# Kernel tuning notes

Hardware: AMD Instinct MI355X
Metric: run time of the kernel (lower is better)

## Reference

```python
import jax, jax.numpy as jnp
import numpy as np

N_NODES = 50000
N_EDGES = 800000
IN_DIM = 4
HID = 64
N_LAYERS = 3
BN_EPS = 1e-5


def setup_inputs() -> dict:
    key = jax.random.key(0)
    ks = jax.random.split(key, 16)
    x = jax.random.normal(ks[0], (N_NODES, IN_DIM), dtype=jnp.float32)
    edge_index = jax.random.randint(ks[1], (2, N_EDGES), 0, N_NODES, dtype=jnp.int32)
    # input projection
    W_in = jax.random.normal(ks[2], (IN_DIM, HID), dtype=jnp.float32) * 0.1
    b_in = jnp.zeros((HID,), dtype=jnp.float32)
    # stacked per-layer GCN weights and BatchNorm (eval-mode) params
    conv_w = jax.random.normal(ks[3], (N_LAYERS, HID, HID), dtype=jnp.float32) * 0.1
    conv_b = jnp.zeros((N_LAYERS, HID), dtype=jnp.float32)
    bn_gamma = jnp.ones((N_LAYERS, HID), dtype=jnp.float32)
    bn_beta = jnp.zeros((N_LAYERS, HID), dtype=jnp.float32)
    bn_mean = jax.random.normal(ks[4], (N_LAYERS, HID), dtype=jnp.float32) * 0.01
    bn_var = jnp.abs(jax.random.normal(ks[5], (N_LAYERS, HID), dtype=jnp.float32)) * 0.1 + 1.0
    # output projection: Linear(HID,HID) -> ReLU -> Dropout(eval: identity) -> Linear(HID,OUT)
    W1 = jax.random.normal(ks[6], (HID, HID), dtype=jnp.float32) * 0.1
    b1 = jnp.zeros((HID,), dtype=jnp.float32)
    W2 = jax.random.normal(ks[7], (HID, IN_DIM), dtype=jnp.float32) * 0.01  # xavier gain 0.1
    b2 = jnp.zeros((IN_DIM,), dtype=jnp.float32)
    return {
        "x": x, "edge_index": edge_index,
        "W_in": W_in, "b_in": b_in,
        "conv_w": conv_w, "conv_b": conv_b,
        "bn_gamma": bn_gamma, "bn_beta": bn_beta,
        "bn_mean": bn_mean, "bn_var": bn_var,
        "W1": W1, "b1": b1, "W2": W2, "b2": b2,
    }


def _gcn_graph(edge_index, n_nodes):
    """Add self loops and compute symmetric GCN normalization per edge."""
    loops = jnp.arange(n_nodes, dtype=edge_index.dtype)
    src = jnp.concatenate([edge_index[0], loops])
    dst = jnp.concatenate([edge_index[1], loops])
    deg = jax.ops.segment_sum(jnp.ones_like(dst, dtype=jnp.float32), dst,
                              num_segments=n_nodes)  # in-degree incl. self loop
    dinv = jax.lax.rsqrt(jnp.maximum(deg, 1e-12))
    enorm = dinv[src] * dinv[dst]  # [E+N]
    return src, dst, enorm


def reference(x, edge_index, W_in, b_in, conv_w, conv_b, bn_gamma, bn_beta,
              bn_mean, bn_var, W1, b1, W2, b2):
    n = x.shape[0]
    src, dst, enorm = _gcn_graph(edge_index, n)

    input_x = x
    h = x @ W_in + b_in  # [N, HID]
    for i in range(N_LAYERS):
        residual = h
        # GCNConv: linear -> normalized gather/scatter aggregate -> bias
        hw = h @ conv_w[i]
        msg = hw[src] * enorm[:, None]  # [E+N, HID] irregular gather
        h = jax.ops.segment_sum(msg, dst, num_segments=n) + conv_b[i]
        # BatchNorm1d (eval) + ReLU (dropout is identity in eval)
        h = (h - bn_mean[i]) * jax.lax.rsqrt(bn_var[i] + BN_EPS) * bn_gamma[i] + bn_beta[i]
        h = jax.nn.relu(h)
        h = h + residual  # shapes always match (HID == HID)
    # output projection MLP
    delta = jax.nn.relu(h @ W1 + b1) @ W2 + b2  # [N, IN_DIM]
    return input_x + delta
```

## Files before the change

### kernel.cpp

```cpp
#include <hip/hip_runtime.h>

#define HID 64
#define CAP 64

__device__ __forceinline__ float bf2f(unsigned short u) {
    return __uint_as_float(((unsigned)u) << 16);
}
__device__ __forceinline__ unsigned short f2bf(float f) {
    unsigned u = __float_as_uint(f);
    u += 0x7FFF + ((u >> 16) & 1);
    return (unsigned short)(u >> 16);
}

__global__ void fill_gemm(const int* __restrict__ eidx, int* __restrict__ cursor,
                          int* __restrict__ col, int E, int n, int nodes_per,
                          int chunk, int fillBlocks,
                          const float* __restrict__ x, const float* __restrict__ Win,
                          const float* __restrict__ bin, const float* __restrict__ W,
                          float* __restrict__ h, float* __restrict__ hw0) {
    if (blockIdx.x < fillBlocks) {
        int p = blockIdx.x & 7;
        int q = blockIdx.x >> 3;
        const int* __restrict__ dst = eidx + E;
        int lo = p * nodes_per;
        int hi = lo + nodes_per;
        int beg = q * chunk;
        int end = min(beg + chunk, E);
        for (int e = beg + threadIdx.x; e < end; e += 256) {
            int d = dst[e];
            if (d >= lo && d < hi) {
                int s = eidx[e];
                int pos = atomicAdd(&cursor[d], 1);
                if (pos < CAP) col[(d << 6) + pos] = s;
            }
        }
        return;
    }
    __shared__ float wl[64 * 64];
    __shared__ float winl[256];
    __shared__ float binl[64];
    __shared__ float hl[256];
    int b = blockIdx.x - fillBlocks;
    int tid = threadIdx.x;
#pragma unroll
    for (int i = 0; i < 16; ++i) wl[tid + 256 * i] = W[tid + 256 * i];
    winl[tid] = Win[tid];
    if (tid < 64) binl[tid] = bin[tid];
    int j = tid & 63;
    int w = tid >> 6;
    for (int c = 0; c < 8; ++c) {
        int v = b * 32 + c * 4 + w;
        __syncthreads();
        float hv = 0.f;
        if (v < n) {
            float4 xv = *(const float4*)&x[(size_t)v * 4];
            hv = binl[j] + xv.x * winl[j] + xv.y * winl[64 + j]
                         + xv.z * winl[128 + j] + xv.w * winl[192 + j];
            h[(size_t)v * 64 + j] = hv;
        }
        hl[tid] = hv;
        __syncthreads();
        if (v < n) {
            const float* hr = &hl[w * 64];
            float acc = 0.f;
#pragma unroll
            for (int k = 0; k < 64; ++k) acc += hr[k] * wl[k * 64 + j];
            hw0[(size_t)v * 64 + j] = acc;
        }
    }
}

__global__ void scale_k(const int* __restrict__ cursor, const float* __restrict__ hw0,
                        unsigned short* __restrict__ hws0, float* __restrict__ dinv,
                        int n) {
    int t = threadIdx.x;
    int v = blockIdx.x * 16 + (t >> 4);
    int gl = t & 15;
    if (v >= n) return;
    float di = rsqrtf((float)cursor[v] + 1.0f);
    if (gl == 0) dinv[v] = di;
    float4 a = *(const float4*)&hw0[(size_t)v * 64 + gl * 4];
    ushort4 o;
    o.x = f2bf(a.x * di);
    o.y = f2bf(a.y * di);
    o.z = f2bf(a.z * di);
    o.w = f2bf(a.w * di);
    *(ushort4*)&hws0[(size_t)v * 64 + gl * 4] = o;
}

#define GATHER_BODY(hws4, col, beg, end, s0, s1, s2, s3, gl)                      \
    {                                                                             \
        int e = beg;                                                              \
        for (; e + 7 < end; e += 8) {                                             \
            int c0 = col[e], c1 = col[e+1], c2 = col[e+2], c3 = col[e+3];         \
            int c4 = col[e+4], c5 = col[e+5], c6 = col[e+6], c7 = col[e+7];       \
            ushort4 m0 = hws4[(size_t)c0 * 16 + gl];                              \
            ushort4 m1 = hws4[(size_t)c1 * 16 + gl];                              \
            ushort4 m2 = hws4[(size_t)c2 * 16 + gl];                              \
            ushort4 m3 = hws4[(size_t)c3 * 16 + gl];                              \
            ushort4 m4 = hws4[(size_t)c4 * 16 + gl];                              \
            ushort4 m5 = hws4[(size_t)c5 * 16 + gl];                              \
            ushort4 m6 = hws4[(size_t)c6 * 16 + gl];                              \
            ushort4 m7 = hws4[(size_t)c7 * 16 + gl];                              \
            s0 += bf2f(m0.x)+bf2f(m1.x)+bf2f(m2.x)+bf2f(m3.x)                     \
                + bf2f(m4.x)+bf2f(m5.x)+bf2f(m6.x)+bf2f(m7.x);                    \
            s1 += bf2f(m0.y)+bf2f(m1.y)+bf2f(m2.y)+bf2f(m3.y)                     \
                + bf2f(m4.y)+bf2f(m5.y)+bf2f(m6.y)+bf2f(m7.y);                    \
            s2 += bf2f(m0.z)+bf2f(m1.z)+bf2f(m2.z)+bf2f(m3.z)                     \
                + bf2f(m4.z)+bf2f(m5.z)+bf2f(m6.z)+bf2f(m7.z);                    \
            s3 += bf2f(m0.w)+bf2f(m1.w)+bf2f(m2.w)+bf2f(m3.w)                     \
                + bf2f(m4.w)+bf2f(m5.w)+bf2f(m6.w)+bf2f(m7.w);                    \
        }                                                                         \
        for (; e + 3 < end; e += 4) {                                             \
            int c0 = col[e], c1 = col[e+1], c2 = col[e+2], c3 = col[e+3];         \
            ushort4 m0 = hws4[(size_t)c0 * 16 + gl];                              \
            ushort4 m1 = hws4[(size_t)c1 * 16 + gl];                              \
            ushort4 m2 = hws4[(size_t)c2 * 16 + gl];                              \
            ushort4 m3 = hws4[(size_t)c3 * 16 + gl];                              \
            s0 += bf2f(m0.x)+bf2f(m1.x)+bf2f(m2.x)+bf2f(m3.x);                    \
            s1 += bf2f(m0.y)+bf2f(m1.y)+bf2f(m2.y)+bf2f(m3.y);                    \
            s2 += bf2f(m0.z)+bf2f(m1.z)+bf2f(m2.z)+bf2f(m3.z);                    \
            s3 += bf2f(m0.w)+bf2f(m1.w)+bf2f(m2.w)+bf2f(m3.w);                    \
        }                                                                         \
        for (; e < end; ++e) {                                                    \
            ushort4 me = hws4[(size_t)col[e] * 16 + gl];                          \
            s0 += bf2f(me.x); s1 += bf2f(me.y); s2 += bf2f(me.z); s3 += bf2f(me.w);\
        }                                                                         \
    }

__global__ void gather_gemm(const int* __restrict__ cursor, const int* __restrict__ col,
                            const unsigned short* __restrict__ hws_in,
                            const float* __restrict__ dinv, float* __restrict__ h,
                            const float* __restrict__ cb, const float* __restrict__ gamma,
                            const float* __restrict__ beta, const float* __restrict__ mean,
                            const float* __restrict__ var, const float* __restrict__ Wn,
                            unsigned short* __restrict__ hws_out, int n) {
    __shared__ float wl[64 * 64];
    __shared__ float hl[16 * 64];
    int tid = threadIdx.x;
#pragma unroll
    for (int i = 0; i < 16; ++i) wl[tid + 256 * i] = Wn[tid + 256 * i];
    int lane = tid & 63, wave = tid >> 6;
    int grp = lane >> 4, gl = lane & 15;
    int ln = wave * 4 + grp;
    int v = blockIdx.x * 16 + ln;
    bool valid = v < n;
    int vv = valid ? v : 0;
    int j0 = gl * 4;
    const ushort4* hws4 = (const ushort4*)hws_in;
    ushort4 m = hws4[(size_t)vv * 16 + gl];
    float s0 = bf2f(m.x), s1 = bf2f(m.y), s2 = bf2f(m.z), s3 = bf2f(m.w);
    int beg = vv << 6;
    int end = beg + (valid ? min(cursor[vv], CAP) : 0);
    GATHER_BODY(hws4, col, beg, end, s0, s1, s2, s3, gl)
    float di = dinv[vv];
    float4 cbv = *(const float4*)&cb[j0];
    float4 mnv = *(const float4*)&mean[j0];
    float4 vrv = *(const float4*)&var[j0];
    float4 gmv = *(const float4*)&gamma[j0];
    float4 btv = *(const float4*)&beta[j0];
    float4 hres = *(const float4*)&h[(size_t)vv * 64 + j0];
    float4 o;
    o.x = fmaxf((s0 * di + cbv.x - mnv.x) * rsqrtf(vrv.x + 1e-5f) * gmv.x + btv.x, 0.f) + hres.x;
    o.y = fmaxf((s1 * di + cbv.y - mnv.y) * rsqrtf(vrv.y + 1e-5f) * gmv.y + btv.y, 0.f) + hres.y;
    o.z = fmaxf((s2 * di + cbv.z - mnv.z) * rsqrtf(vrv.z + 1e-5f) * gmv.z + btv.z, 0.f) + hres.z;
    o.w = fmaxf((s3 * di + cbv.w - mnv.w) * rsqrtf(vrv.w + 1e-5f) * gmv.w + btv.w, 0.f) + hres.w;
    if (valid) *(float4*)&h[(size_t)vv * 64 + j0] = o;
    *(float4*)&hl[ln * 64 + j0] = o;
    __syncthreads();
    int j = lane;
    for (int c = 0; c < 4; ++c) {
        int ln2 = wave * 4 + c;
        int v2 = blockIdx.x * 16 + ln2;
        if (v2 < n) {
            const float* hr = &hl[ln2 * 64];
            float acc = 0.f;
#pragma unroll
            for (int k = 0; k < 64; ++k) acc += hr[k] * wl[k * 64 + j];
            hws_out[(size_t)v2 * 64 + j] = f2bf(acc * dinv[v2]);
        }
    }
}

__global__ void gather_mlp(const int* __restrict__ cursor, const int* __restrict__ col,
                           const unsigned short* __restrict__ hws_in,
                           const float* __restrict__ dinv, const float* __restrict__ h,
                           const float* __restrict__ cb, const float* __restrict__ gamma,
                           const float* __restrict__ beta, const float* __restrict__ mean,
                           const float* __restrict__ var, const float* __restrict__ x,
                           const float* __restrict__ W1, const float* __restrict__ b1,
                           const float* __restrict__ W2, const float* __restrict__ b2,
                           float* __restrict__ out, int n) {
    __shared__ float wl[64 * 64];
    __shared__ float w2l[256];
    __shared__ float hl[16 * 64];
    __shared__ float tl[16 * 68];
    int tid = threadIdx.x;
#pragma unroll
    for (int i = 0; i < 16; ++i) wl[tid + 256 * i] = W1[tid + 256 * i];
    w2l[tid] = W2[tid];
    int lane = tid & 63, wave = tid >> 6;
    int grp = lane >> 4, gl = lane & 15;
    int ln = wave * 4 + grp;
    int v = blockIdx.x * 16 + ln;
    bool valid = v < n;
    int vv = valid ? v : 0;
    int j0 = gl * 4;
    const ushort4* hws4 = (const ushort4*)hws_in;
    ushort4 m = hws4[(size_t)vv * 16 + gl];
    float s0 = bf2f(m.x), s1 = bf2f(m.y), s2 = bf2f(m.z), s3 = bf2f(m.w);
    int beg = vv << 6;
    int end = beg + (valid ? min(cursor[vv], CAP) : 0);
    GATHER_BODY(hws4, col, beg, end, s0, s1, s2, s3, gl)
    float di = dinv[vv];
    float4 cbv = *(const float4*)&cb[j0];
    float4 mnv = *(const float4*)&mean[j0];
    float4 vrv = *(const float4*)&var[j0];
    float4 gmv = *(const float4*)&gamma[j0];
    float4 btv = *(const float4*)&beta[j0];
    float4 hres = *(const float4*)&h[(size_t)vv * 64 + j0];
    float4 o;
    o.x = fmaxf((s0 * di + cbv.x - mnv.x) * rsqrtf(vrv.x + 1e-5f) * gmv.x + btv.x, 0.f) + hres.x;
    o.y = fmaxf((s1 * di + cbv.y - mnv.y) * rsqrtf(vrv.y + 1e-5f) * gmv.y + btv.y, 0.f) + hres.y;
    o.z = fmaxf((s2 * di + cbv.z - mnv.z) * rsqrtf(vrv.z + 1e-5f) * gmv.z + btv.z, 0.f) + hres.z;
    o.w = fmaxf((s3 * di + cbv.w - mnv.w) * rsqrtf(vrv.w + 1e-5f) * gmv.w + btv.w, 0.f) + hres.w;
    *(float4*)&hl[ln * 64 + j0] = o;
    __syncthreads();
    int j = lane;
    float b1j = b1[j];
    for (int c = 0; c < 4; ++c) {
        int ln2 = wave * 4 + c;
        const float* hr = &hl[ln2 * 64];
        float acc = b1j;
#pragma unroll
        for (int k = 0; k < 64; ++k) acc += hr[k] * wl[k * 64 + j];
        tl[ln2 * 68 + j] = fmaxf(acc, 0.f);
    }
    __syncthreads();
    if (tid < 64) {
        int ln2 = tid >> 2, mm = tid & 3;
        int v2 = blockIdx.x * 16 + ln2;
        if (v2 < n) {
            const float* tr = &tl[ln2 * 68];
            float acc = b2[mm];
#pragma unroll
            for (int k = 0; k < 64; ++k) acc += tr[k] * w2l[k * 4 + mm];
            out[(size_t)v2 * 4 + mm] = x[(size_t)v2 * 4 + mm] + acc;
        }
    }
}

extern "C" void kernel_launch(void* const* d_in, const int* in_sizes, int n_in,
                              void* d_out, int out_size, void* d_ws, size_t ws_size,
                              hipStream_t stream) {
    const float* x     = (const float*)d_in[0];
    const int*   eidx  = (const int*)  d_in[1];
    const float* Win   = (const float*)d_in[2];
    const float* bin   = (const float*)d_in[3];
    const float* convw = (const float*)d_in[4];
    const float* convb = (const float*)d_in[5];
    const float* gamma = (const float*)d_in[6];
    const float* beta  = (const float*)d_in[7];
    const float* mean  = (const float*)d_in[8];
    const float* var   = (const float*)d_in[9];
    const float* W1    = (const float*)d_in[10];
    const float* b1    = (const float*)d_in[11];
    const float* W2    = (const float*)d_in[12];
    const float* b2    = (const float*)d_in[13];
    float* out = (float*)d_out;

    int n = in_sizes[0] / 4;
    int E = in_sizes[1] / 2;
    const int B = 256;

    char* p = (char*)d_ws;
    size_t nh = (size_t)n * 64;
    float*          dinv   = (float*)p;          p += ((size_t)n + 16) * 4;
    float*          h      = (float*)p;          p += nh * 4;
    float*          hw0    = (float*)p;          p += nh * 4;
    unsigned short* hws0   = (unsigned short*)p; p += nh * 2;
    unsigned short* hws1   = (unsigned short*)p; p += nh * 2;
    int*            cursor = (int*)p;            p += ((size_t)n + 16) * 4;
    int*            col    = (int*)p;            p += (size_t)n * CAP * 4;

    const int GP = 128;
    int fillBlocks = GP * 8;
    int nodes_per = (n + 7) / 8;
    int chunk = (E + GP - 1) / GP;

    hipMemsetAsync(cursor, 0, (size_t)n * 4, stream);
    int NB32 = (n + 31) / 32;
    fill_gemm<<<fillBlocks + NB32, B, 0, stream>>>(
        eidx, cursor, col, E, n, nodes_per, chunk, fillBlocks,
        x, Win, bin, convw, h, hw0);

    int NB16 = (n + 15) / 16;
    scale_k<<<NB16, B, 0, stream>>>(cursor, hw0, hws0, dinv, n);

    gather_gemm<<<NB16, B, 0, stream>>>(cursor, col, hws0, dinv, h,
        convb, gamma, beta, mean, var, convw + 4096, hws1, n);
    gather_gemm<<<NB16, B, 0, stream>>>(cursor, col, hws1, dinv, h,
        convb + 64, gamma + 64, beta + 64, mean + 64, var + 64, convw + 8192, hws0, n);
    gather_mlp<<<NB16, B, 0, stream>>>(cursor, col, hws0, dinv, h,
        convb + 128, gamma + 128, beta + 128, mean + 128, var + 128,
        x, W1, b1, W2, b2, out, n);
}
```

Measured before the change: 236.9 us.

## Drop scale kernel by applying source degree norm inside gather; vectorize fill

Removes the separate scale kernel and the fp32 hw0 buffer. Features are now stored unscaled in bf16, and each gather looks up the source node's degree and applies rsqrt(deg+1) per edge with an FMA, so the dinv array goes away. The CSR fill loop also reads destination indices as int4, with the chunk size rounded up to a multiple of 4. The cost is an extra random cursor load and rsqrt per edge in all three gather passes, traded for one fewer launch and less global traffic.

```diff
diff --git a/kernel.cpp b/kernel.cpp
--- a/kernel.cpp
+++ b/kernel.cpp
@@ -17,7 +17,7 @@
                           int chunk, int fillBlocks,
                           const float* __restrict__ x, const float* __restrict__ Win,
                           const float* __restrict__ bin, const float* __restrict__ W,
-                          float* __restrict__ h, float* __restrict__ hw0) {
+                          float* __restrict__ h, unsigned short* __restrict__ hws0) {
     if (blockIdx.x < fillBlocks) {
         int p = blockIdx.x & 7;
         int q = blockIdx.x >> 3;
@@ -26,7 +26,31 @@
         int hi = lo + nodes_per;
         int beg = q * chunk;
         int end = min(beg + chunk, E);
-        for (int e = beg + threadIdx.x; e < end; e += 256) {
+        int vend = beg + ((end - beg) & ~3);
+        for (int e = beg + threadIdx.x * 4; e < vend; e += 1024) {
+            int4 dv = *(const int4*)&dst[e];
+            if (dv.x >= lo && dv.x < hi) {
+                int s = eidx[e];
+                int pos = atomicAdd(&cursor[dv.x], 1);
+                if (pos < CAP) col[(dv.x << 6) + pos] = s;
+            }
+            if (dv.y >= lo && dv.y < hi) {
+                int s = eidx[e + 1];
+                int pos = atomicAdd(&cursor[dv.y], 1);
+                if (pos < CAP) col[(dv.y << 6) + pos] = s;
+            }
+            if (dv.z >= lo && dv.z < hi) {
+                int s = eidx[e + 2];
+                int pos = atomicAdd(&cursor[dv.z], 1);
+                if (pos < CAP) col[(dv.z << 6) + pos] = s;
+            }
+            if (dv.w >= lo && dv.w < hi) {
+                int s = eidx[e + 3];
+                int pos = atomicAdd(&cursor[dv.w], 1);
+                if (pos < CAP) col[(dv.w << 6) + pos] = s;
+            }
+        }
+        for (int e = vend + threadIdx.x; e < end; e += 256) {
             int d = dst[e];
             if (d >= lo && d < hi) {
                 int s = eidx[e];
@@ -65,35 +89,25 @@
             float acc = 0.f;
 #pragma unroll
             for (int k = 0; k < 64; ++k) acc += hr[k] * wl[k * 64 + j];
-            hw0[(size_t)v * 64 + j] = acc;
-        }
-    }
-}
-
-__global__ void scale_k(const int* __restrict__ cursor, const float* __restrict__ hw0,
-                        unsigned short* __restrict__ hws0, float* __restrict__ dinv,
-                        int n) {
-    int t = threadIdx.x;
-    int v = blockIdx.x * 16 + (t >> 4);
-    int gl = t & 15;
-    if (v >= n) return;
-    float di = rsqrtf((float)cursor[v] + 1.0f);
-    if (gl == 0) dinv[v] = di;
-    float4 a = *(const float4*)&hw0[(size_t)v * 64 + gl * 4];
-    ushort4 o;
-    o.x = f2bf(a.x * di);
-    o.y = f2bf(a.y * di);
-    o.z = f2bf(a.z * di);
-    o.w = f2bf(a.w * di);
-    *(ushort4*)&hws0[(size_t)v * 64 + gl * 4] = o;
-}
-
-#define GATHER_BODY(hws4, col, beg, end, s0, s1, s2, s3, gl)                      \
+            hws0[(size_t)v * 64 + j] = f2bf(acc);
+        }
+    }
+}
+
+#define GATHER_BODY(hws4, col, cursor, beg, end, s0, s1, s2, s3, gl)              \
     {                                                                             \
         int e = beg;                                                              \
         for (; e + 7 < end; e += 8) {                                             \
             int c0 = col[e], c1 = col[e+1], c2 = col[e+2], c3 = col[e+3];         \
             int c4 = col[e+4], c5 = col[e+5], c6 = col[e+6], c7 = col[e+7];       \
+            float d0 = rsqrtf((float)cursor[c0] + 1.0f);                          \
+            float d1 = rsqrtf((float)cursor[c1] + 1.0f);                          \
+            float d2 = rsqrtf((float)cursor[c2] + 1.0f);                          \
+            float d3 = rsqrtf((float)cursor[c3] + 1.0f);                          \
+            float d4 = rsqrtf((float)cursor[c4] + 1.0f);                          \
+            float d5 = rsqrtf((float)cursor[c5] + 1.0f);                          \
+            float d6 = rsqrtf((float)cursor[c6] + 1.0f);                          \
+            float d7 = rsqrtf((float)cursor[c7] + 1.0f);                          \
             ushort4 m0 = hws4[(size_t)c0 * 16 + gl];                              \
             ushort4 m1 = hws4[(size_t)c1 * 16 + gl];                              \
             ushort4 m2 = hws4[(size_t)c2 * 16 + gl];                              \
@@ -102,35 +116,54 @@
             ushort4 m5 = hws4[(size_t)c5 * 16 + gl];                              \
             ushort4 m6 = hws4[(size_t)c6 * 16 + gl];                              \
             ushort4 m7 = hws4[(size_t)c7 * 16 + gl];                              \
-            s0 += bf2f(m0.x)+bf2f(m1.x)+bf2f(m2.x)+bf2f(m3.x)                     \
-                + bf2f(m4.x)+bf2f(m5.x)+bf2f(m6.x)+bf2f(m7.x);                    \
-            s1 += bf2f(m0.y)+bf2f(m1.y)+bf2f(m2.y)+bf2f(m3.y)                     \
-                + bf2f(m4.y)+bf2f(m5.y)+bf2f(m6.y)+bf2f(m7.y);                    \
-            s2 += bf2f(m0.z)+bf2f(m1.z)+bf2f(m2.z)+bf2f(m3.z)                     \
-                + bf2f(m4.z)+bf2f(m5.z)+bf2f(m6.z)+bf2f(m7.z);                    \
-            s3 += bf2f(m0.w)+bf2f(m1.w)+bf2f(m2.w)+bf2f(m3.w)                     \
-                + bf2f(m4.w)+bf2f(m5.w)+bf2f(m6.w)+bf2f(m7.w);                    \
+            s0 = fmaf(bf2f(m0.x), d0, s0); s0 = fmaf(bf2f(m1.x), d1, s0);         \
+            s0 = fmaf(bf2f(m2.x), d2, s0); s0 = fmaf(bf2f(m3.x), d3, s0);         \
+            s0 = fmaf(bf2f(m4.x), d4, s0); s0 = fmaf(bf2f(m5.x), d5, s0);         \
+            s0 = fmaf(bf2f(m6.x), d6, s0); s0 = fmaf(bf2f(m7.x), d7, s0);         \
+            s1 = fmaf(bf2f(m0.y), d0, s1); s1 = fmaf(bf2f(m1.y), d1, s1);         \
+            s1 = fmaf(bf2f(m2.y), d2, s1); s1 = fmaf(bf2f(m3.y), d3, s1);         \
+            s1 = fmaf(bf2f(m4.y), d4, s1); s1 = fmaf(bf2f(m5.y), d5, s1);         \
+            s1 = fmaf(bf2f(m6.y), d6, s1); s1 = fmaf(bf2f(m7.y), d7, s1);         \
+            s2 = fmaf(bf2f(m0.z), d0, s2); s2 = fmaf(bf2f(m1.z), d1, s2);         \
+            s2 = fmaf(bf2f(m2.z), d2, s2); s2 = fmaf(bf2f(m3.z), d3, s2);         \
+            s2 = fmaf(bf2f(m4.z), d4, s2); s2 = fmaf(bf2f(m5.z), d5, s2);         \
+            s2 = fmaf(bf2f(m6.z), d6, s2); s2 = fmaf(bf2f(m7.z), d7, s2);         \
+            s3 = fmaf(bf2f(m0.w), d0, s3); s3 = fmaf(bf2f(m1.w), d1, s3);         \
+            s3 = fmaf(bf2f(m2.w), d2, s3); s3 = fmaf(bf2f(m3.w), d3, s3);         \
+            s3 = fmaf(bf2f(m4.w), d4, s3); s3 = fmaf(bf2f(m5.w), d5, s3);         \
+            s3 = fmaf(bf2f(m6.w), d6, s3); s3 = fmaf(bf2f(m7.w), d7, s3);         \
         }                                                                         \
         for (; e + 3 < end; e += 4) {                                             \
             int c0 = col[e], c1 = col[e+1], c2 = col[e+2], c3 = col[e+3];         \
+            float d0 = rsqrtf((float)cursor[c0] + 1.0f);                          \
+            float d1 = rsqrtf((float)cursor[c1] + 1.0f);                          \
+            float d2 = rsqrtf((float)cursor[c2] + 1.0f);                          \
+            float d3 = rsqrtf((float)cursor[c3] + 1.0f);                          \
             ushort4 m0 = hws4[(size_t)c0 * 16 + gl];                              \
             ushort4 m1 = hws4[(size_t)c1 * 16 + gl];                              \
             ushort4 m2 = hws4[(size_t)c2 * 16 + gl];                              \
             ushort4 m3 = hws4[(size_t)c3 * 16 + gl];                              \
-            s0 += bf2f(m0.x)+bf2f(m1.x)+bf2f(m2.x)+bf2f(m3.x);                    \
-            s1 += bf2f(m0.y)+bf2f(m1.y)+bf2f(m2.y)+bf2f(m3.y);                    \
-            s2 += bf2f(m0.z)+bf2f(m1.z)+bf2f(m2.z)+bf2f(m3.z);                    \
-            s3 += bf2f(m0.w)+bf2f(m1.w)+bf2f(m2.w)+bf2f(m3.w);                    \
+            s0 = fmaf(bf2f(m0.x), d0, s0); s0 = fmaf(bf2f(m1.x), d1, s0);         \
+            s0 = fmaf(bf2f(m2.x), d2, s0); s0 = fmaf(bf2f(m3.x), d3, s0);         \
+            s1 = fmaf(bf2f(m0.y), d0, s1); s1 = fmaf(bf2f(m1.y), d1, s1);         \
+            s1 = fmaf(bf2f(m2.y), d2, s1); s1 = fmaf(bf2f(m3.y), d3, s1);         \
+            s2 = fmaf(bf2f(m0.z), d0, s2); s2 = fmaf(bf2f(m1.z), d1, s2);         \
+            s2 = fmaf(bf2f(m2.z), d2, s2); s2 = fmaf(bf2f(m3.z), d3, s2);         \
+            s3 = fmaf(bf2f(m0.w), d0, s3); s3 = fmaf(bf2f(m1.w), d1, s3);         \
+            s3 = fmaf(bf2f(m2.w), d2, s3); s3 = fmaf(bf2f(m3.w), d3, s3);         \
         }                                                                         \
         for (; e < end; ++e) {                                                    \
-            ushort4 me = hws4[(size_t)col[e] * 16 + gl];                          \
-            s0 += bf2f(me.x); s1 += bf2f(me.y); s2 += bf2f(me.z); s3 += bf2f(me.w);\
+            int c0 = col[e];                                                      \
+            float d0 = rsqrtf((float)cursor[c0] + 1.0f);                          \
+            ushort4 me = hws4[(size_t)c0 * 16 + gl];                              \
+            s0 = fmaf(bf2f(me.x), d0, s0); s1 = fmaf(bf2f(me.y), d0, s1);         \
+            s2 = fmaf(bf2f(me.z), d0, s2); s3 = fmaf(bf2f(me.w), d0, s3);         \
         }                                                                         \
     }
 
 __global__ void gather_gemm(const int* __restrict__ cursor, const int* __restrict__ col,
                             const unsigned short* __restrict__ hws_in,
-                            const float* __restrict__ dinv, float* __restrict__ h,
+                            float* __restrict__ h,
                             const float* __restrict__ cb, const float* __restrict__ gamma,
                             const float* __restrict__ beta, const float* __restrict__ mean,
                             const float* __restrict__ var, const float* __restrict__ Wn,
@@ -148,12 +181,14 @@
     int vv = valid ? v : 0;
     int j0 = gl * 4;
     const ushort4* hws4 = (const ushort4*)hws_in;
+    int cnt = cursor[vv];
+    float di = rsqrtf((float)cnt + 1.0f);
     ushort4 m = hws4[(size_t)vv * 16 + gl];
-    float s0 = bf2f(m.x), s1 = bf2f(m.y), s2 = bf2f(m.z), s3 = bf2f(m.w);
+    float s0 = bf2f(m.x) * di, s1 = bf2f(m.y) * di,
+          s2 = bf2f(m.z) * di, s3 = bf2f(m.w) * di;
     int beg = vv << 6;
-    int end = beg + (valid ? min(cursor[vv], CAP) : 0);
-    GATHER_BODY(hws4, col, beg, end, s0, s1, s2, s3, gl)
-    float di = dinv[vv];
+    int end = beg + (valid ? min(cnt, CAP) : 0);
+    GATHER_BODY(hws4, col, cursor, beg, end, s0, s1, s2, s3, gl)
     float4 cbv = *(const float4*)&cb[j0];
     float4 mnv = *(const float4*)&mean[j0];
     float4 vrv = *(const float4*)&var[j0];
@@ -177,14 +212,14 @@
             float acc = 0.f;
 #pragma unroll
             for (int k = 0; k < 64; ++k) acc += hr[k] * wl[k * 64 + j];
-            hws_out[(size_t)v2 * 64 + j] = f2bf(acc * dinv[v2]);
+            hws_out[(size_t)v2 * 64 + j] = f2bf(acc);
         }
     }
 }
 
 __global__ void gather_mlp(const int* __restrict__ cursor, const int* __restrict__ col,
                            const unsigned short* __restrict__ hws_in,
-                           const float* __restrict__ dinv, const float* __restrict__ h,
+                           const float* __restrict__ h,
                            const float* __restrict__ cb, const float* __restrict__ gamma,
                            const float* __restrict__ beta, const float* __restrict__ mean,
                            const float* __restrict__ var, const float* __restrict__ x,
@@ -207,12 +242,14 @@
     int vv = valid ? v : 0;
     int j0 = gl * 4;
     const ushort4* hws4 = (const ushort4*)hws_in;
+    int cnt = cursor[vv];
+    float di = rsqrtf((float)cnt + 1.0f);
     ushort4 m = hws4[(size_t)vv * 16 + gl];
-    float s0 = bf2f(m.x), s1 = bf2f(m.y), s2 = bf2f(m.z), s3 = bf2f(m.w);
+    float s0 = bf2f(m.x) * di, s1 = bf2f(m.y) * di,
+          s2 = bf2f(m.z) * di, s3 = bf2f(m.w) * di;
     int beg = vv << 6;
-    int end = beg + (valid ? min(cursor[vv], CAP) : 0);
-    GATHER_BODY(hws4, col, beg, end, s0, s1, s2, s3, gl)
-    float di = dinv[vv];
+    int end = beg + (valid ? min(cnt, CAP) : 0);
+    GATHER_BODY(hws4, col, cursor, beg, end, s0, s1, s2, s3, gl)
     float4 cbv = *(const float4*)&cb[j0];
     float4 mnv = *(const float4*)&mean[j0];
     float4 vrv = *(const float4*)&var[j0];
@@ -275,9 +312,7 @@
 
     char* p = (char*)d_ws;
     size_t nh = (size_t)n * 64;
-    float*          dinv   = (float*)p;          p += ((size_t)n + 16) * 4;
     float*          h      = (float*)p;          p += nh * 4;
-    float*          hw0    = (float*)p;          p += nh * 4;
     unsigned short* hws0   = (unsigned short*)p; p += nh * 2;
     unsigned short* hws1   = (unsigned short*)p; p += nh * 2;
     int*            cursor = (int*)p;            p += ((size_t)n + 16) * 4;
@@ -286,22 +321,20 @@
     const int GP = 128;
     int fillBlocks = GP * 8;
     int nodes_per = (n + 7) / 8;
-    int chunk = (E + GP - 1) / GP;
+    int chunk = (((E + GP - 1) / GP) + 3) & ~3;
 
     hipMemsetAsync(cursor, 0, (size_t)n * 4, stream);
     int NB32 = (n + 31) / 32;
     fill_gemm<<<fillBlocks + NB32, B, 0, stream>>>(
         eidx, cursor, col, E, n, nodes_per, chunk, fillBlocks,
-        x, Win, bin, convw, h, hw0);
+        x, Win, bin, convw, h, hws0);
 
     int NB16 = (n + 15) / 16;
-    scale_k<<<NB16, B, 0, stream>>>(cursor, hw0, hws0, dinv, n);
-
-    gather_gemm<<<NB16, B, 0, stream>>>(cursor, col, hws0, dinv, h,
+    gather_gemm<<<NB16, B, 0, stream>>>(cursor, col, hws0, h,
         convb, gamma, beta, mean, var, convw + 4096, hws1, n);
-    gather_gemm<<<NB16, B, 0, stream>>>(cursor, col, hws1, dinv, h,
+    gather_gemm<<<NB16, B, 0, stream>>>(cursor, col, hws1, h,
         convb + 64, gamma + 64, beta + 64, mean + 64, var + 64, convw + 8192, hws0, n);
-    gather_mlp<<<NB16, B, 0, stream>>>(cursor, col, hws0, dinv, h,
+    gather_mlp<<<NB16, B, 0, stream>>>(cursor, col, hws0, h,
         convb + 128, gamma + 128, beta + 128, mean + 128, var + 128,
         x, W1, b1, W2, b2, out, n);
 }
```

Measured after the change: 233.2 us. No clear change (-1.6%).
